# Kernel optimization log

Hardware: AMD Instinct MI355X
Metric: run time of the kernel (lower is better)

Reference implementation:

```python
import jax, jax.numpy as jnp
import numpy as np

B, C, L = 32, 64, 4096
PS, STRIDE = 16, 8
PC = (L - PS) // STRIDE + 1  # 511
HID = 64


def setup_inputs() -> dict:
    key = jax.random.key(0)
    k = jax.random.split(key, 5)
    X = jax.random.normal(k[0], (B, C, L), dtype=jnp.float32)
    W1 = jax.random.normal(k[1], (HID, PS), dtype=jnp.float32) * 0.05  # Conv1d(1,64,PS) weight
    b1 = jax.random.normal(k[2], (HID,), dtype=jnp.float32) * 0.05
    W2 = jax.random.normal(k[3], (2, HID), dtype=jnp.float32) * 0.05   # Conv1d(64,2,1) weight
    b2 = jax.random.normal(k[4], (2,), dtype=jnp.float32) * 0.05
    return {"X": X, "W1": W1, "b1": b1, "W2": W2, "b2": b2}


def reference(X, W1, b1, W2, b2):
    Bn, Cn, Ln = X.shape
    s_bias = (PS - 1) / 2.0
    # anchors: center of each patch along the sequence axis
    anchor = jnp.arange(PC, dtype=X.dtype) * STRIDE + 0.5 * (PS - 1)  # (PC,)

    # ---- OffsetPredictor: unfold into (B, C, PC, PS) sliding windows ----
    idx = jnp.arange(PC)[:, None] * STRIDE + jnp.arange(PS)[None, :]  # (PC, PS)
    patches = X[:, :, idx]  # (B, C, PC, PS)
    # Conv1d(1, HID, PS) over a length-PS window == dense matmul with W1
    h = jax.nn.gelu(jnp.einsum('bcps,ks->bcpk', patches, W1) + b1, approximate=False)
    off = jnp.einsum('bcpk,jk->bcpj', h, W2) + b2  # (B, C, PC, 2)
    off = off.transpose(0, 2, 1, 3)  # (B, PC, C, 2)

    # ---- BoxCoder.decode ----
    dx = off[..., 0]
    ds = jax.nn.relu(off[..., 1] + s_bias)
    ref = anchor[None, :, None]
    lo = jnp.clip((dx + ref - ds) / (Ln - 1), 0.0, 1.0)  # (B, PC, C)
    hi = jnp.clip((dx + ref + ds) / (Ln - 1), 0.0, 1.0)

    # ---- BoxCoder.meshgrid: linear interp from box endpoints (align_corners) ----
    t = jnp.arange(PS, dtype=X.dtype) / (PS - 1)  # (PS,)
    xs = lo[..., None] + (hi - lo)[..., None] * t  # (B, PC, C, PS), in [0,1]
    ys = jnp.arange(Cn, dtype=X.dtype) / (Cn - 1)  # (C,), in [0,1]

    # ---- grid_sample(img=(B,1,C,L), grid=(xs,ys)*2-1, bilinear, align_corners=True) ----
    ix = xs * (Ln - 1)                                            # (B, PC, C, PS)
    iy = jnp.broadcast_to(ys[None, None, :, None] * (Cn - 1), ix.shape)
    ix0 = jnp.floor(ix)
    iy0 = jnp.floor(iy)
    wx = ix - ix0
    wy = iy - iy0
    ix0i = jnp.clip(ix0.astype(jnp.int32), 0, Ln - 1)
    ix1i = jnp.clip(ix0i + 1, 0, Ln - 1)
    iy0i = jnp.clip(iy0.astype(jnp.int32), 0, Cn - 1)
    iy1i = jnp.clip(iy0i + 1, 0, Cn - 1)

    gather = jax.vmap(lambda x, r, c: x[r, c])  # over batch; x:(C,L)
    v00 = gather(X, iy0i, ix0i)
    v01 = gather(X, iy0i, ix1i)
    v10 = gather(X, iy1i, ix0i)
    v11 = gather(X, iy1i, ix1i)
    out = (v00 * (1 - wx) + v01 * wx) * (1 - wy) + (v10 * (1 - wx) + v11 * wx) * wy
    # (B, PC, C, PS) -> (B, C, PC, PS)
    return out.transpose(0, 2, 1, 3)
```

## Files before the change

kernel.cpp:

```cpp
#include <hip/hip_runtime.h>
#include <math.h>

#define L_    4096
#define PS_   16
#define STR_  8
#define PC_   511
#define HID_  64
#define NBLK_ 2048

__device__ __forceinline__ float gelu_as(float x) {
    float az = fabsf(x) * 0.70710678118654752440f;
    float d  = fmaf(0.3275911f, az, 1.0f);
    float t  = __builtin_amdgcn_rcpf(d);
    float p  = fmaf(1.061405429f, t, -1.453152027f);
    p = fmaf(p, t, 1.421413741f);
    p = fmaf(p, t, -0.284496736f);
    p = fmaf(p, t, 0.254829592f);
    p = p * t;
    float e  = __builtin_amdgcn_exp2f(az * az * -1.4426950408889634f);
    float r  = fmaf(-p, e, 1.0f);
    r = copysignf(r, x);
    float h = 0.5f * x;
    return fmaf(h, r, h);
}

__device__ __forceinline__ void sample_store(const float* __restrict__ s_row,
                                             float* __restrict__ outp,
                                             int p, float dx, float ds) {
    const float refp = (float)(p * STR_) + 7.5f;
    const float d2   = fmaxf(ds + 7.5f, 0.0f);
    const float a    = dx + refp;
    const float loi  = fminf(fmaxf(a - d2, 0.0f), 4095.0f);
    const float hii  = fminf(fmaxf(a + d2, 0.0f), 4095.0f);
    const float span = hii - loi;

    float4 o[4];
    float* ov = reinterpret_cast<float*>(o);
    #pragma unroll
    for (int s = 0; s < PS_; ++s) {
        float t  = (float)s / 15.0f;
        float ix = fmaf(span, t, loi);
        float f  = floorf(ix);
        float wx = ix - f;
        int i0 = (int)f;
        int i1 = min(i0 + 1, L_ - 1);
        float v0 = s_row[i0];
        float v1 = s_row[i1];
        ov[s] = fmaf(wx, v1 - v0, v0);
    }
    float4* o4 = reinterpret_cast<float4*>(outp);
    #pragma unroll
    for (int i = 0; i < 4; ++i) o4[i] = o[i];
}

__global__ __launch_bounds__(256) void depatch_kernel(
    const float* __restrict__ X,
    const float* __restrict__ W1,
    const float* __restrict__ b1,
    const float* __restrict__ W2,
    const float* __restrict__ b2,
    float* __restrict__ out)
{
    __shared__ float s_row[L_];

    const int tid = threadIdx.x;
    const int bc  = blockIdx.x;
    const float* xrow = X + (size_t)bc * L_;

    {
        const float4* src4 = reinterpret_cast<const float4*>(xrow);
        float4* dst4 = reinterpret_cast<float4*>(s_row);
        #pragma unroll
        for (int i = 0; i < 4; ++i) dst4[tid + 256 * i] = src4[tid + 256 * i];
    }
    __syncthreads();

    const int p0  = tid;
    const int p1  = tid + 256;
    const int p1c = (p1 < PC_) ? p1 : (PC_ - 1);

    float pa[PS_], pb[PS_];
    {
        const float4* ra = reinterpret_cast<const float4*>(s_row + p0  * STR_);
        const float4* rb = reinterpret_cast<const float4*>(s_row + p1c * STR_);
        #pragma unroll
        for (int i = 0; i < 4; ++i) {
            float4 va = ra[i], vb = rb[i];
            pa[4*i+0]=va.x; pa[4*i+1]=va.y; pa[4*i+2]=va.z; pa[4*i+3]=va.w;
            pb[4*i+0]=vb.x; pb[4*i+1]=vb.y; pb[4*i+2]=vb.z; pb[4*i+3]=vb.w;
        }
    }

    float dxa = b2[0], dsa = b2[1];
    float dxb = dxa,  dsb = dsa;

    #pragma unroll 4
    for (int k = 0; k < HID_; ++k) {
        const float* w = W1 + k * PS_;
        float acca = b1[k];
        float accb = acca;
        #pragma unroll
        for (int s = 0; s < PS_; ++s) {
            float ws = w[s];
            acca = fmaf(pa[s], ws, acca);
            accb = fmaf(pb[s], ws, accb);
        }
        float ga = gelu_as(acca);
        float gb = gelu_as(accb);
        float w20 = W2[k], w21 = W2[HID_ + k];
        dxa = fmaf(ga, w20, dxa);  dsa = fmaf(ga, w21, dsa);
        dxb = fmaf(gb, w20, dxb);  dsb = fmaf(gb, w21, dsb);
    }

    float* obase = out + (size_t)bc * PC_ * PS_;
    sample_store(s_row, obase + (size_t)p0 * PS_, p0, dxa, dsa);
    if (p1 < PC_)
        sample_store(s_row, obase + (size_t)p1 * PS_, p1, dxb, dsb);
}

extern "C" void kernel_launch(void* const* d_in, const int* in_sizes, int n_in,
                              void* d_out, int out_size, void* d_ws, size_t ws_size,
                              hipStream_t stream) {
    const float* X  = (const float*)d_in[0];
    const float* W1 = (const float*)d_in[1];
    const float* b1 = (const float*)d_in[2];
    const float* W2 = (const float*)d_in[3];
    const float* b2 = (const float*)d_in[4];
    float* out = (float*)d_out;

    depatch_kernel<<<dim3(NBLK_), dim3(256), 0, stream>>>(X, W1, b1, W2, b2, out);
}
```

Baseline: 146.7 us.

## Compute patch MLP with bf16 MFMA and polynomial GELU, reduce via shuffles

Moves the per-patch 16x64 first-layer matmul from scalar FMAs onto bf16 MFMA 16x16x32 instructions, using a bf16 copy of the row in shared memory. The erf-based GELU is replaced with a clamped odd polynomial, and the second layer is reduced across lanes with xor shuffles into shared dx/ds arrays before sampling. This cuts ALU work in the compute-bound MLP stage. In exchange it loses precision: bf16 inputs and weights plus the approximate GELU could perturb offsets enough to shift floor() indices in the sampling step.

```diff
diff --git a/kernel.cpp b/kernel.cpp
--- a/kernel.cpp
+++ b/kernel.cpp
@@ -8,18 +8,21 @@
 #define HID_  64
 #define NBLK_ 2048
 
-__device__ __forceinline__ float gelu_as(float x) {
-    float az = fabsf(x) * 0.70710678118654752440f;
-    float d  = fmaf(0.3275911f, az, 1.0f);
-    float t  = __builtin_amdgcn_rcpf(d);
-    float p  = fmaf(1.061405429f, t, -1.453152027f);
-    p = fmaf(p, t, 1.421413741f);
-    p = fmaf(p, t, -0.284496736f);
-    p = fmaf(p, t, 0.254829592f);
-    p = p * t;
-    float e  = __builtin_amdgcn_exp2f(az * az * -1.4426950408889634f);
-    float r  = fmaf(-p, e, 1.0f);
-    r = copysignf(r, x);
+typedef __bf16 bf16x8 __attribute__((ext_vector_type(8)));
+typedef float  f32x4  __attribute__((ext_vector_type(4)));
+
+__device__ __forceinline__ float gelu_poly(float x) {
+    float u = x * x;
+    float p = fmaf(u, 4.5473e-9f,    -8.2448e-8f);
+    p = fmaf(p, u,  1.33194e-6f);
+    p = fmaf(p, u, -1.8889343e-5f);
+    p = fmaf(p, u,  2.3087745e-4f);
+    p = fmaf(p, u, -2.3746734e-3f);
+    p = fmaf(p, u,  1.9947114e-2f);
+    p = fmaf(p, u, -1.3298076e-1f);
+    p = fmaf(p, u,  7.9788456e-1f);
+    float r = x * p;
+    r = fminf(fmaxf(r, -1.0f), 1.0f);
     float h = 0.5f * x;
     return fmaf(h, r, h);
 }
@@ -61,7 +64,10 @@
     const float* __restrict__ b2,
     float* __restrict__ out)
 {
-    __shared__ float s_row[L_];
+    __shared__ float  s_row[L_];
+    __shared__ __attribute__((aligned(16))) __bf16 s_rowh[L_ + 32];
+    __shared__ float  s_dx[512];
+    __shared__ float  s_ds[512];
 
     const int tid = threadIdx.x;
     const int bc  = blockIdx.x;
@@ -71,51 +77,90 @@
         const float4* src4 = reinterpret_cast<const float4*>(xrow);
         float4* dst4 = reinterpret_cast<float4*>(s_row);
         #pragma unroll
-        for (int i = 0; i < 4; ++i) dst4[tid + 256 * i] = src4[tid + 256 * i];
+        for (int i = 0; i < 4; ++i) {
+            float4 v = src4[tid + 256 * i];
+            dst4[tid + 256 * i] = v;
+            union { __bf16 h[4]; unsigned long long u; } pk;
+            pk.h[0] = (__bf16)v.x; pk.h[1] = (__bf16)v.y;
+            pk.h[2] = (__bf16)v.z; pk.h[3] = (__bf16)v.w;
+            *reinterpret_cast<unsigned long long*>(&s_rowh[(tid + 256 * i) * 4]) = pk.u;
+        }
+        if (tid < 32) s_rowh[L_ + tid] = (__bf16)0.0f;
+    }
+
+    const int l  = tid & 63;
+    const int lr = l & 15;
+    const int lkb = (l >> 4) * 8;
+
+    bf16x8 bfrag[4];
+    float  b1v[4], w2x[4], w2s[4];
+    #pragma unroll
+    for (int nb = 0; nb < 4; ++nb) {
+        #pragma unroll
+        for (int j = 0; j < 8; ++j) {
+            int ks = lkb + j;
+            float w = (ks < PS_) ? W1[(nb * 16 + lr) * PS_ + ks] : 0.0f;
+            bfrag[nb][j] = (__bf16)w;
+        }
+        b1v[nb] = b1[nb * 16 + lr];
+        w2x[nb] = W2[nb * 16 + lr];
+        w2s[nb] = W2[HID_ + nb * 16 + lr];
     }
     __syncthreads();
 
-    const int p0  = tid;
-    const int p1  = tid + 256;
-    const int p1c = (p1 < PC_) ? p1 : (PC_ - 1);
+    const int wave = tid >> 6;
+    const f32x4 zacc = {0.0f, 0.0f, 0.0f, 0.0f};
+    for (int gi = 0; gi < 8; ++gi) {
+        const int g  = wave * 8 + gi;
+        const int pb = g * 16;
+        const bf16x8 a = *reinterpret_cast<const bf16x8*>(&s_rowh[(pb + lr + (l >> 4)) * 8]);
+        f32x4 c0 = __builtin_amdgcn_mfma_f32_16x16x32_bf16(a, bfrag[0], zacc, 0, 0, 0);
+        f32x4 c1 = __builtin_amdgcn_mfma_f32_16x16x32_bf16(a, bfrag[1], zacc, 0, 0, 0);
+        f32x4 c2 = __builtin_amdgcn_mfma_f32_16x16x32_bf16(a, bfrag[2], zacc, 0, 0, 0);
+        f32x4 c3 = __builtin_amdgcn_mfma_f32_16x16x32_bf16(a, bfrag[3], zacc, 0, 0, 0);
 
-    float pa[PS_], pb[PS_];
-    {
-        const float4* ra = reinterpret_cast<const float4*>(s_row + p0  * STR_);
-        const float4* rb = reinterpret_cast<const float4*>(s_row + p1c * STR_);
+        float dxp[4], dsp[4];
         #pragma unroll
-        for (int i = 0; i < 4; ++i) {
-            float4 va = ra[i], vb = rb[i];
-            pa[4*i+0]=va.x; pa[4*i+1]=va.y; pa[4*i+2]=va.z; pa[4*i+3]=va.w;
-            pb[4*i+0]=vb.x; pb[4*i+1]=vb.y; pb[4*i+2]=vb.z; pb[4*i+3]=vb.w;
+        for (int r = 0; r < 4; ++r) {
+            float g0 = gelu_poly(c0[r] + b1v[0]);
+            float g1 = gelu_poly(c1[r] + b1v[1]);
+            float g2 = gelu_poly(c2[r] + b1v[2]);
+            float g3 = gelu_poly(c3[r] + b1v[3]);
+            float dx = g0 * w2x[0];
+            dx = fmaf(g1, w2x[1], dx);
+            dx = fmaf(g2, w2x[2], dx);
+            dx = fmaf(g3, w2x[3], dx);
+            float ds = g0 * w2s[0];
+            ds = fmaf(g1, w2s[1], ds);
+            ds = fmaf(g2, w2s[2], ds);
+            ds = fmaf(g3, w2s[3], ds);
+            #pragma unroll
+            for (int off = 1; off < 16; off <<= 1) {
+                dx += __shfl_xor(dx, off, 64);
+                ds += __shfl_xor(ds, off, 64);
+            }
+            dxp[r] = dx; dsp[r] = ds;
+        }
+        if (lr == 0) {
+            const int p0w = pb + (l >> 4) * 4;
+            #pragma unroll
+            for (int r = 0; r < 4; ++r) {
+                s_dx[p0w + r] = dxp[r];
+                s_ds[p0w + r] = dsp[r];
+            }
         }
     }
+    __syncthreads();
 
-    float dxa = b2[0], dsa = b2[1];
-    float dxb = dxa,  dsb = dsa;
+    const float b20 = b2[0];
+    const float b21 = b2[1];
+    float* obase = out + (size_t)bc * PC_ * PS_;
 
-    #pragma unroll 4
-    for (int k = 0; k < HID_; ++k) {
-        const float* w = W1 + k * PS_;
-        float acca = b1[k];
-        float accb = acca;
-        #pragma unroll
-        for (int s = 0; s < PS_; ++s) {
-            float ws = w[s];
-            acca = fmaf(pa[s], ws, acca);
-            accb = fmaf(pb[s], ws, accb);
-        }
-        float ga = gelu_as(acca);
-        float gb = gelu_as(accb);
-        float w20 = W2[k], w21 = W2[HID_ + k];
-        dxa = fmaf(ga, w20, dxa);  dsa = fmaf(ga, w21, dsa);
-        dxb = fmaf(gb, w20, dxb);  dsb = fmaf(gb, w21, dsb);
-    }
-
-    float* obase = out + (size_t)bc * PC_ * PS_;
-    sample_store(s_row, obase + (size_t)p0 * PS_, p0, dxa, dsa);
+    const int p0 = tid;
+    sample_store(s_row, obase + (size_t)p0 * PS_, p0, s_dx[p0] + b20, s_ds[p0] + b21);
+    const int p1 = tid + 256;
     if (p1 < PC_)
-        sample_store(s_row, obase + (size_t)p1 * PS_, p1, dxb, dsb);
+        sample_store(s_row, obase + (size_t)p1 * PS_, p1, s_dx[p1] + b20, s_ds[p1] + b21);
 }
 
 extern "C" void kernel_launch(void* const* d_in, const int* in_sizes, int n_in,
```

After: 142.9 us. -2.6%, faster.
